# Kernel tuning notes

Hardware: AMD Instinct MI355X
Metric: run time of the kernel (lower is better)

Reference implementation:

```python
import jax, jax.numpy as jnp
import numpy as np
from jax import lax

ITERATIONS = 10
B, I, D, J, E = 512, 7, 512, 64, 128


def setup_inputs() -> dict:
    key = jax.random.key(0)
    k1, k2, k3 = jax.random.split(key, 3)
    f_bid = jax.random.normal(k1, (B, I, D), dtype=jnp.float32)
    p_bi = jax.random.uniform(k2, (B, I), dtype=jnp.float32)
    weights = jax.random.normal(k3, (I, D, J, E), dtype=jnp.float32)
    return {"f_bid": f_bid, "p_bi": p_bi, "weights": weights}


def reference(f_bid, p_bi, weights):
    # Precompute the per-capsule vote tensor once: [B, I, J, E]
    f_W_bije = jnp.einsum('bid,idje->bije', f_bid, weights)
    b = f_bid.shape[0]
    j, e = weights.shape[2], weights.shape[3]
    c0 = jnp.ones((b, j, e), dtype=f_bid.dtype)

    def body(c_bj, _):
        # routing logits over output capsules j, softmax over j (dim=-1 of 'bij')
        r_bij = jax.nn.softmax(jnp.einsum('bije,bje->bij', f_W_bije, c_bj), axis=-1)
        c_next = jnp.einsum('bi,bij,bije->bje', p_bi, r_bij, f_W_bije)
        return c_next, r_bij

    c_bj, r_stack = lax.scan(body, c0, None, length=ITERATIONS)
    return c_bj, r_stack[-1]
```

## Files before the change

### kernel.cpp

```cpp
#include <hip/hip_runtime.h>
#include <hip/hip_bf16.h>

#define B_SZ 512
#define I_SZ 7
#define D_SZ 512
#define J_SZ 64
#define E_SZ 128
#define N_SZ 8192
#define ITERS 10

typedef __attribute__((ext_vector_type(8))) short bf16x8;
typedef __attribute__((ext_vector_type(4))) float f32x4;

#define AST 40
#define BST 40

#if defined(__has_builtin)
#if __has_builtin(__builtin_amdgcn_cvt_pk_bf16_f32)
#define HAVE_CVT_PK_BF16 1
#endif
#endif

__device__ inline void split2(float x0, float x1, unsigned& hp, unsigned& lp) {
#ifdef HAVE_CVT_PK_BF16
    auto h = __builtin_amdgcn_cvt_pk_bf16_f32(x0, x1);
    hp = __builtin_bit_cast(unsigned, h);
    union { unsigned u; float f; } b0, b1;
    b0.u = hp << 16;
    b1.u = hp & 0xFFFF0000u;
    auto l = __builtin_amdgcn_cvt_pk_bf16_f32(x0 - b0.f, x1 - b1.f);
    lp = __builtin_bit_cast(unsigned, l);
#else
    union { float f; unsigned u; } u0, u1;
    u0.f = x0; u1.f = x1;
    unsigned r0 = u0.u + 0x7FFF + ((u0.u >> 16) & 1);
    unsigned r1 = u1.u + 0x7FFF + ((u1.u >> 16) & 1);
    hp = __builtin_amdgcn_perm(r1, r0, 0x07060302);
    union { unsigned u; float f; } h0, h1;
    h0.u = r0 & 0xFFFF0000u;
    h1.u = r1 & 0xFFFF0000u;
    union { float f; unsigned u; } s0, s1;
    s0.f = x0 - h0.f; s1.f = x1 - h1.f;
    unsigned q0 = s0.u + 0x7FFF + ((s0.u >> 16) & 1);
    unsigned q1 = s1.u + 0x7FFF + ((s1.u >> 16) & 1);
    lp = __builtin_amdgcn_perm(q1, q0, 0x07060302);
#endif
}

__global__ __launch_bounds__(256) void vote_gemm_mfma(
    const float* __restrict__ f,
    const float* __restrict__ W,
    float* __restrict__ fW)
{
    const int i  = blockIdx.z;
    const int m0 = blockIdx.y * 128;
    const int n0 = blockIdx.x * 128;
    const int th = threadIdx.x;

    __shared__ short As_hi[128 * AST], As_lo[128 * AST];
    __shared__ short Bs_hi[128 * BST], Bs_lo[128 * BST];

    const int am  = th >> 1;
    const int akg = th & 1;
    const int bn  = th & 127;
    const int bkh = th >> 7;

    const float* fA = f + (size_t)(m0 + am) * (I_SZ * D_SZ) + (size_t)i * D_SZ + akg * 16;
    const float* WB = W + (size_t)i * D_SZ * N_SZ + n0 + bn;

    const int wave = th >> 6, lane = th & 63;
    const int wr = wave >> 1, wc = wave & 1;
    const int lm = lane & 15, quad = lane >> 4;

    f32x4 acc[4][4];
#pragma unroll
    for (int a = 0; a < 4; ++a)
#pragma unroll
        for (int c = 0; c < 4; ++c)
            acc[a][c] = (f32x4){0.f, 0.f, 0.f, 0.f};

    float av[16], bv[16];
    {
        float4 t0 = *(const float4*)(fA);
        float4 t1 = *(const float4*)(fA + 4);
        float4 t2 = *(const float4*)(fA + 8);
        float4 t3 = *(const float4*)(fA + 12);
        av[0]=t0.x; av[1]=t0.y; av[2]=t0.z; av[3]=t0.w;
        av[4]=t1.x; av[5]=t1.y; av[6]=t1.z; av[7]=t1.w;
        av[8]=t2.x; av[9]=t2.y; av[10]=t2.z; av[11]=t2.w;
        av[12]=t3.x; av[13]=t3.y; av[14]=t3.z; av[15]=t3.w;
        const float* pb = WB + (size_t)(bkh * 16) * N_SZ;
#pragma unroll
        for (int r = 0; r < 16; ++r) bv[r] = pb[(size_t)r * N_SZ];
    }

    for (int k0 = 0; k0 < D_SZ; k0 += 32) {
        uint4 ah0, al0, ah1, al1, bh0, bl0, bh1, bl1;
        split2(av[0],  av[1],  ah0.x, al0.x);
        split2(av[2],  av[3],  ah0.y, al0.y);
        split2(av[4],  av[5],  ah0.z, al0.z);
        split2(av[6],  av[7],  ah0.w, al0.w);
        split2(av[8],  av[9],  ah1.x, al1.x);
        split2(av[10], av[11], ah1.y, al1.y);
        split2(av[12], av[13], ah1.z, al1.z);
        split2(av[14], av[15], ah1.w, al1.w);
        split2(bv[0],  bv[1],  bh0.x, bl0.x);
        split2(bv[2],  bv[3],  bh0.y, bl0.y);
        split2(bv[4],  bv[5],  bh0.z, bl0.z);
        split2(bv[6],  bv[7],  bh0.w, bl0.w);
        split2(bv[8],  bv[9],  bh1.x, bl1.x);
        split2(bv[10], bv[11], bh1.y, bl1.y);
        split2(bv[12], bv[13], bh1.z, bl1.z);
        split2(bv[14], bv[15], bh1.w, bl1.w);

        __syncthreads();
        *(uint4*)&As_hi[am * AST + akg * 16]     = ah0;
        *(uint4*)&As_hi[am * AST + akg * 16 + 8] = ah1;
        *(uint4*)&As_lo[am * AST + akg * 16]     = al0;
        *(uint4*)&As_lo[am * AST + akg * 16 + 8] = al1;
        *(uint4*)&Bs_hi[bn * BST + bkh * 16]     = bh0;
        *(uint4*)&Bs_hi[bn * BST + bkh * 16 + 8] = bh1;
        *(uint4*)&Bs_lo[bn * BST + bkh * 16]     = bl0;
        *(uint4*)&Bs_lo[bn * BST + bkh * 16 + 8] = bl1;
        __syncthreads();

        if (k0 + 32 < D_SZ) {
            const float* pa = fA + k0 + 32;
            float4 t0 = *(const float4*)(pa);
            float4 t1 = *(const float4*)(pa + 4);
            float4 t2 = *(const float4*)(pa + 8);
            float4 t3 = *(const float4*)(pa + 12);
            av[0]=t0.x; av[1]=t0.y; av[2]=t0.z; av[3]=t0.w;
            av[4]=t1.x; av[5]=t1.y; av[6]=t1.z; av[7]=t1.w;
            av[8]=t2.x; av[9]=t2.y; av[10]=t2.z; av[11]=t2.w;
            av[12]=t3.x; av[13]=t3.y; av[14]=t3.z; av[15]=t3.w;
            const float* pb = WB + (size_t)(k0 + 32 + bkh * 16) * N_SZ;
#pragma unroll
            for (int r = 0; r < 16; ++r) bv[r] = pb[(size_t)r * N_SZ];
        }

        bf16x8 Ah[4], Al[4], Bh[4], Bl[4];
#pragma unroll
        for (int t = 0; t < 4; ++t) {
            const int ar = (wr * 64 + t * 16 + lm) * AST + quad * 8;
            Ah[t] = *(const bf16x8*)&As_hi[ar];
            Al[t] = *(const bf16x8*)&As_lo[ar];
            const int br = (wc * 64 + t * 16 + lm) * BST + quad * 8;
            Bh[t] = *(const bf16x8*)&Bs_hi[br];
            Bl[t] = *(const bf16x8*)&Bs_lo[br];
        }
#pragma unroll
        for (int tm = 0; tm < 4; ++tm)
#pragma unroll
            for (int tn = 0; tn < 4; ++tn) {
                acc[tm][tn] = __builtin_amdgcn_mfma_f32_16x16x32_bf16(Ah[tm], Bh[tn], acc[tm][tn], 0, 0, 0);
                acc[tm][tn] = __builtin_amdgcn_mfma_f32_16x16x32_bf16(Ah[tm], Bl[tn], acc[tm][tn], 0, 0, 0);
                acc[tm][tn] = __builtin_amdgcn_mfma_f32_16x16x32_bf16(Al[tm], Bh[tn], acc[tm][tn], 0, 0, 0);
            }
    }

#pragma unroll
    for (int tm = 0; tm < 4; ++tm) {
        const int rowb = m0 + wr * 64 + tm * 16 + quad * 4;
#pragma unroll
        for (int tn = 0; tn < 4; ++tn) {
            const int col = n0 + wc * 64 + tn * 16 + lm;
#pragma unroll
            for (int r = 0; r < 4; ++r)
                fW[((size_t)(rowb + r) * I_SZ + i) * N_SZ + col] = acc[tm][tn][r];
        }
    }
}

__global__ __launch_bounds__(1024) void routing_kernel(
    const float* __restrict__ fW,
    const float* __restrict__ p,
    float* __restrict__ c_out,
    float* __restrict__ r_out)
{
    const int b   = blockIdx.x;
    const int tid = threadIdx.x;
    const int j   = tid >> 4;
    const int sub = tid & 15;

    __shared__ float G_sh[64][49];
    __shared__ float s_sh[64][9];
    __shared__ float w_sh[2][64][9];
    __shared__ float p_sh[8];

    if (tid < I_SZ) p_sh[tid] = p[(size_t)b * I_SZ + tid];

    float4 fw[I_SZ][2];
    const float* base = fW + (size_t)b * I_SZ * N_SZ + j * E_SZ + sub * 8;
#pragma unroll
    for (int i = 0; i < I_SZ; ++i) {
        fw[i][0] = *(const float4*)(base + (size_t)i * N_SZ);
        fw[i][1] = *(const float4*)(base + (size_t)i * N_SZ + 4);
    }

#pragma unroll
    for (int i = 0; i < I_SZ; ++i) {
        float s = fw[i][0].x + fw[i][0].y + fw[i][0].z + fw[i][0].w
                + fw[i][1].x + fw[i][1].y + fw[i][1].z + fw[i][1].w;
        s += __shfl_xor(s, 1); s += __shfl_xor(s, 2);
        s += __shfl_xor(s, 4); s += __shfl_xor(s, 8);
        if (sub == 0) s_sh[j][i] = s;
#pragma unroll
        for (int i2 = i; i2 < I_SZ; ++i2) {
            float g = fw[i][0].x * fw[i2][0].x + fw[i][0].y * fw[i2][0].y
                    + fw[i][0].z * fw[i2][0].z + fw[i][0].w * fw[i2][0].w
                    + fw[i][1].x * fw[i2][1].x + fw[i][1].y * fw[i2][1].y
                    + fw[i][1].z * fw[i2][1].z + fw[i][1].w * fw[i2][1].w;
            g += __shfl_xor(g, 1); g += __shfl_xor(g, 2);
            g += __shfl_xor(g, 4); g += __shfl_xor(g, 8);
            if (sub == 0) { G_sh[j][i * 7 + i2] = g; G_sh[j][i2 * 7 + i] = g; }
        }
    }
    __syncthreads();

    for (int t = 0; t < ITERS; ++t) {
        if (tid < I_SZ * 64) {
            const int ii = tid >> 6;
            const int jj = tid & 63;
            float l;
            if (t == 0) {
                l = s_sh[jj][ii];
            } else {
                const int rb = t & 1;
                l = 0.f;
#pragma unroll
                for (int i2 = 0; i2 < I_SZ; ++i2)
                    l = fmaf(w_sh[rb][jj][i2], G_sh[jj][ii * 7 + i2], l);
            }
            float mx = l;
#pragma unroll
            for (int off = 32; off > 0; off >>= 1)
                mx = fmaxf(mx, __shfl_xor(mx, off));
            float ex = __expf(l - mx);
            float sm = ex;
#pragma unroll
            for (int off = 32; off > 0; off >>= 1)
                sm += __shfl_xor(sm, off);
            float r = ex / sm;
            if (t == ITERS - 1)
                r_out[(size_t)b * (I_SZ * J_SZ) + ii * 64 + jj] = r;
            w_sh[(t + 1) & 1][jj][ii] = p_sh[ii] * r;
        }
        __syncthreads();
    }

    float4 a0 = make_float4(0.f, 0.f, 0.f, 0.f);
    float4 a1 = make_float4(0.f, 0.f, 0.f, 0.f);
#pragma unroll
    for (int i = 0; i < I_SZ; ++i) {
        float wv = w_sh[ITERS & 1][j][i];
        a0.x = fmaf(wv, fw[i][0].x, a0.x); a0.y = fmaf(wv, fw[i][0].y, a0.y);
        a0.z = fmaf(wv, fw[i][0].z, a0.z); a0.w = fmaf(wv, fw[i][0].w, a0.w);
        a1.x = fmaf(wv, fw[i][1].x, a1.x); a1.y = fmaf(wv, fw[i][1].y, a1.y);
        a1.z = fmaf(wv, fw[i][1].z, a1.z); a1.w = fmaf(wv, fw[i][1].w, a1.w);
    }
    float* dst = c_out + (size_t)b * N_SZ + j * E_SZ + sub * 8;
    *(float4*)(dst)     = a0;
    *(float4*)(dst + 4) = a1;
}

extern "C" void kernel_launch(void* const* d_in, const int* in_sizes, int n_in,
                              void* d_out, int out_size, void* d_ws, size_t ws_size,
                              hipStream_t stream) {
    const float* f = (const float*)d_in[0];
    const float* p = (const float*)d_in[1];
    const float* W = (const float*)d_in[2];
    float* out = (float*)d_out;
    float* fW  = (float*)d_ws;

    vote_gemm_mfma<<<dim3(N_SZ / 128, B_SZ / 128, I_SZ), 256, 0, stream>>>(f, W, fW);
    routing_kernel<<<B_SZ, 1024, 0, stream>>>(fW, p, out, out + (size_t)B_SZ * N_SZ);
}
```

Before: 295.0 us.

## Restructure vote GEMM with direct-to-LDS double-buffered loads and larger tiles

The vote GEMM now stages raw fp32 A and B tiles straight from global memory into LDS with global_load_lds, double-buffered and swizzled to avoid bank conflicts. The bf16 hi/lo split moves to after the LDS reads, and block tiles grow to 256x256 with 512 threads. MFMA sections are wrapped in s_setprio. The goal is to overlap global loads with MFMA work and cut register staging and per-step synchronisation. In exchange, the split is repeated by every wave that reads the same tile, and the grid shrinks to 448 large blocks using about 128KB of LDS each, which risks tail imbalance and low occupancy.

```diff
diff --git a/kernel.cpp b/kernel.cpp
--- a/kernel.cpp
+++ b/kernel.cpp
@@ -11,9 +11,6 @@
 
 typedef __attribute__((ext_vector_type(8))) short bf16x8;
 typedef __attribute__((ext_vector_type(4))) float f32x4;
-
-#define AST 40
-#define BST 40
 
 #if defined(__has_builtin)
 #if __has_builtin(__builtin_amdgcn_cvt_pk_bf16_f32)
@@ -47,127 +44,137 @@
 #endif
 }
 
-__global__ __launch_bounds__(256) void vote_gemm_mfma(
+__device__ inline void gload16(const float* g, float* l) {
+    __builtin_amdgcn_global_load_lds(
+        (const __attribute__((address_space(1))) void*)g,
+        (__attribute__((address_space(3))) void*)l, 16, 0, 0);
+}
+
+__global__ __launch_bounds__(512) void vote_gemm_mfma(
     const float* __restrict__ f,
     const float* __restrict__ W,
     float* __restrict__ fW)
 {
     const int i  = blockIdx.z;
-    const int m0 = blockIdx.y * 128;
-    const int n0 = blockIdx.x * 128;
+    const int m0 = blockIdx.y * 256;
+    const int n0 = blockIdx.x * 256;
     const int th = threadIdx.x;
-
-    __shared__ short As_hi[128 * AST], As_lo[128 * AST];
-    __shared__ short Bs_hi[128 * BST], Bs_lo[128 * BST];
-
-    const int am  = th >> 1;
-    const int akg = th & 1;
-    const int bn  = th & 127;
-    const int bkh = th >> 7;
-
-    const float* fA = f + (size_t)(m0 + am) * (I_SZ * D_SZ) + (size_t)i * D_SZ + akg * 16;
-    const float* WB = W + (size_t)i * D_SZ * N_SZ + n0 + bn;
-
-    const int wave = th >> 6, lane = th & 63;
-    const int wr = wave >> 1, wc = wave & 1;
-    const int lm = lane & 15, quad = lane >> 4;
-
-    f32x4 acc[4][4];
-#pragma unroll
-    for (int a = 0; a < 4; ++a)
+    const int lane = th & 63;
+    const int wave = th >> 6;
+    const int wr  = wave >> 2;
+    const int wc  = wave & 3;
+    const int q   = lane >> 4;
+    const int l15 = lane & 15;
+
+    __shared__ float ldsA[2][256 * 32];
+    __shared__ float ldsB[2][32 * 256];
+
+    const float* aSrc[4];
+    const float* bSrc[4];
+#pragma unroll
+    for (int ci = 0; ci < 4; ++ci) {
+        const int ia = ci * 512 + th;
+        const int mA = ia >> 3, sA = ia & 7;
+        aSrc[ci] = f + (size_t)(m0 + mA) * (I_SZ * D_SZ) + (size_t)i * D_SZ
+                     + ((sA ^ (mA & 7)) << 2);
+        const int ib = ci * 512 + th;
+        const int kB = ib >> 6, cB = ib & 63;
+        bSrc[ci] = W + (size_t)i * D_SZ * N_SZ + (size_t)kB * N_SZ + n0
+                     + ((cB ^ ((kB & 8) >> 1)) << 2);
+    }
+
+    auto stage = [&](int slot) {
+#pragma unroll
+        for (int ci = 0; ci < 4; ++ci)
+            gload16(aSrc[ci], &ldsA[slot][(ci * 512 + th) * 4]);
+#pragma unroll
+        for (int ci = 0; ci < 4; ++ci)
+            gload16(bSrc[ci], &ldsB[slot][(ci * 512 + th) * 4]);
+#pragma unroll
+        for (int ci = 0; ci < 4; ++ci) {
+            aSrc[ci] += 32;
+            bSrc[ci] += (size_t)32 * N_SZ;
+        }
+    };
+
+    f32x4 acc[8][4];
+#pragma unroll
+    for (int a = 0; a < 8; ++a)
 #pragma unroll
         for (int c = 0; c < 4; ++c)
             acc[a][c] = (f32x4){0.f, 0.f, 0.f, 0.f};
 
-    float av[16], bv[16];
-    {
-        float4 t0 = *(const float4*)(fA);
-        float4 t1 = *(const float4*)(fA + 4);
-        float4 t2 = *(const float4*)(fA + 8);
-        float4 t3 = *(const float4*)(fA + 12);
-        av[0]=t0.x; av[1]=t0.y; av[2]=t0.z; av[3]=t0.w;
-        av[4]=t1.x; av[5]=t1.y; av[6]=t1.z; av[7]=t1.w;
-        av[8]=t2.x; av[9]=t2.y; av[10]=t2.z; av[11]=t2.w;
-        av[12]=t3.x; av[13]=t3.y; av[14]=t3.z; av[15]=t3.w;
-        const float* pb = WB + (size_t)(bkh * 16) * N_SZ;
-#pragma unroll
-        for (int r = 0; r < 16; ++r) bv[r] = pb[(size_t)r * N_SZ];
-    }
-
-    for (int k0 = 0; k0 < D_SZ; k0 += 32) {
-        uint4 ah0, al0, ah1, al1, bh0, bl0, bh1, bl1;
-        split2(av[0],  av[1],  ah0.x, al0.x);
-        split2(av[2],  av[3],  ah0.y, al0.y);
-        split2(av[4],  av[5],  ah0.z, al0.z);
-        split2(av[6],  av[7],  ah0.w, al0.w);
-        split2(av[8],  av[9],  ah1.x, al1.x);
-        split2(av[10], av[11], ah1.y, al1.y);
-        split2(av[12], av[13], ah1.z, al1.z);
-        split2(av[14], av[15], ah1.w, al1.w);
-        split2(bv[0],  bv[1],  bh0.x, bl0.x);
-        split2(bv[2],  bv[3],  bh0.y, bl0.y);
-        split2(bv[4],  bv[5],  bh0.z, bl0.z);
-        split2(bv[6],  bv[7],  bh0.w, bl0.w);
-        split2(bv[8],  bv[9],  bh1.x, bl1.x);
-        split2(bv[10], bv[11], bh1.y, bl1.y);
-        split2(bv[12], bv[13], bh1.z, bl1.z);
-        split2(bv[14], bv[15], bh1.w, bl1.w);
-
-        __syncthreads();
-        *(uint4*)&As_hi[am * AST + akg * 16]     = ah0;
-        *(uint4*)&As_hi[am * AST + akg * 16 + 8] = ah1;
-        *(uint4*)&As_lo[am * AST + akg * 16]     = al0;
-        *(uint4*)&As_lo[am * AST + akg * 16 + 8] = al1;
-        *(uint4*)&Bs_hi[bn * BST + bkh * 16]     = bh0;
-        *(uint4*)&Bs_hi[bn * BST + bkh * 16 + 8] = bh1;
-        *(uint4*)&Bs_lo[bn * BST + bkh * 16]     = bl0;
-        *(uint4*)&Bs_lo[bn * BST + bkh * 16 + 8] = bl1;
-        __syncthreads();
-
-        if (k0 + 32 < D_SZ) {
-            const float* pa = fA + k0 + 32;
-            float4 t0 = *(const float4*)(pa);
-            float4 t1 = *(const float4*)(pa + 4);
-            float4 t2 = *(const float4*)(pa + 8);
-            float4 t3 = *(const float4*)(pa + 12);
-            av[0]=t0.x; av[1]=t0.y; av[2]=t0.z; av[3]=t0.w;
-            av[4]=t1.x; av[5]=t1.y; av[6]=t1.z; av[7]=t1.w;
-            av[8]=t2.x; av[9]=t2.y; av[10]=t2.z; av[11]=t2.w;
-            av[12]=t3.x; av[13]=t3.y; av[14]=t3.z; av[15]=t3.w;
-            const float* pb = WB + (size_t)(k0 + 32 + bkh * 16) * N_SZ;
-#pragma unroll
-            for (int r = 0; r < 16; ++r) bv[r] = pb[(size_t)r * N_SZ];
-        }
-
-        bf16x8 Ah[4], Al[4], Bh[4], Bl[4];
-#pragma unroll
-        for (int t = 0; t < 4; ++t) {
-            const int ar = (wr * 64 + t * 16 + lm) * AST + quad * 8;
-            Ah[t] = *(const bf16x8*)&As_hi[ar];
-            Al[t] = *(const bf16x8*)&As_lo[ar];
-            const int br = (wc * 64 + t * 16 + lm) * BST + quad * 8;
-            Bh[t] = *(const bf16x8*)&Bs_hi[br];
-            Bl[t] = *(const bf16x8*)&Bs_lo[br];
-        }
-#pragma unroll
-        for (int tm = 0; tm < 4; ++tm)
-#pragma unroll
-            for (int tn = 0; tn < 4; ++tn) {
-                acc[tm][tn] = __builtin_amdgcn_mfma_f32_16x16x32_bf16(Ah[tm], Bh[tn], acc[tm][tn], 0, 0, 0);
-                acc[tm][tn] = __builtin_amdgcn_mfma_f32_16x16x32_bf16(Ah[tm], Bl[tn], acc[tm][tn], 0, 0, 0);
-                acc[tm][tn] = __builtin_amdgcn_mfma_f32_16x16x32_bf16(Al[tm], Bh[tn], acc[tm][tn], 0, 0, 0);
+    stage(0);
+    stage(1);
+    asm volatile("s_waitcnt vmcnt(8)" ::: "memory");
+    __builtin_amdgcn_s_barrier();
+    asm volatile("" ::: "memory");
+
+    for (int t = 0; t < 16; ++t) {
+        const int slot = t & 1;
+        const float* Ab = &ldsA[slot][0];
+        const float* Bb = &ldsB[slot][0];
+
+        uint4 Bh4[4], Bl4[4];
+#pragma unroll
+        for (int ns = 0; ns < 4; ++ns) {
+            const int cs = (wc * 16 + ns * 4 + (l15 >> 2)) ^ ((q & 1) << 2);
+            const float* bp = Bb + q * 8 * 256 + cs * 4 + (l15 & 3);
+            const float b0 = bp[0 * 256], b1 = bp[1 * 256], b2 = bp[2 * 256], b3 = bp[3 * 256];
+            const float b4 = bp[4 * 256], b5 = bp[5 * 256], b6 = bp[6 * 256], b7 = bp[7 * 256];
+            split2(b0, b1, Bh4[ns].x, Bl4[ns].x);
+            split2(b2, b3, Bh4[ns].y, Bl4[ns].y);
+            split2(b4, b5, Bh4[ns].z, Bl4[ns].z);
+            split2(b6, b7, Bh4[ns].w, Bl4[ns].w);
+        }
+
+#pragma unroll
+        for (int ms = 0; ms < 8; ++ms) {
+            const int mrow = wr * 128 + ms * 16 + l15;
+            const int p0 = (q * 2) ^ (l15 & 7);
+            const float4 va = *(const float4*)(Ab + mrow * 32 + ((p0 ^ 0) << 2));
+            const float4 vb = *(const float4*)(Ab + mrow * 32 + ((p0 ^ 1) << 2));
+            uint4 ah, al;
+            split2(va.x, va.y, ah.x, al.x);
+            split2(va.z, va.w, ah.y, al.y);
+            split2(vb.x, vb.y, ah.z, al.z);
+            split2(vb.z, vb.w, ah.w, al.w);
+            const bf16x8 Ah = __builtin_bit_cast(bf16x8, ah);
+            const bf16x8 Al = __builtin_bit_cast(bf16x8, al);
+            __builtin_amdgcn_s_setprio(1);
+#pragma unroll
+            for (int ns = 0; ns < 4; ++ns) {
+                const bf16x8 Bh = __builtin_bit_cast(bf16x8, Bh4[ns]);
+                const bf16x8 Bl = __builtin_bit_cast(bf16x8, Bl4[ns]);
+                acc[ms][ns] = __builtin_amdgcn_mfma_f32_16x16x32_bf16(Ah, Bh, acc[ms][ns], 0, 0, 0);
+                acc[ms][ns] = __builtin_amdgcn_mfma_f32_16x16x32_bf16(Ah, Bl, acc[ms][ns], 0, 0, 0);
+                acc[ms][ns] = __builtin_amdgcn_mfma_f32_16x16x32_bf16(Al, Bh, acc[ms][ns], 0, 0, 0);
             }
-    }
-
-#pragma unroll
-    for (int tm = 0; tm < 4; ++tm) {
-        const int rowb = m0 + wr * 64 + tm * 16 + quad * 4;
-#pragma unroll
-        for (int tn = 0; tn < 4; ++tn) {
-            const int col = n0 + wc * 64 + tn * 16 + lm;
+            __builtin_amdgcn_s_setprio(0);
+        }
+
+        asm volatile("s_waitcnt lgkmcnt(0)" ::: "memory");
+        __builtin_amdgcn_s_barrier();
+        asm volatile("" ::: "memory");
+        if (t < 14) {
+            stage(slot);
+            asm volatile("s_waitcnt vmcnt(8)" ::: "memory");
+        } else {
+            asm volatile("s_waitcnt vmcnt(0)" ::: "memory");
+        }
+        __builtin_amdgcn_s_barrier();
+        asm volatile("" ::: "memory");
+    }
+
+#pragma unroll
+    for (int ms = 0; ms < 8; ++ms) {
+        const int rowb = m0 + wr * 128 + ms * 16 + q * 4;
+#pragma unroll
+        for (int ns = 0; ns < 4; ++ns) {
+            const int col = n0 + wc * 64 + ns * 16 + l15;
 #pragma unroll
             for (int r = 0; r < 4; ++r)
-                fW[((size_t)(rowb + r) * I_SZ + i) * N_SZ + col] = acc[tm][tn][r];
+                fW[((size_t)(rowb + r) * I_SZ + i) * N_SZ + col] = acc[ms][ns][r];
         }
     }
 }
@@ -273,6 +280,6 @@
     float* out = (float*)d_out;
     float* fW  = (float*)d_ws;
 
-    vote_gemm_mfma<<<dim3(N_SZ / 128, B_SZ / 128, I_SZ), 256, 0, stream>>>(f, W, fW);
+    vote_gemm_mfma<<<dim3(N_SZ / 256, B_SZ / 256, I_SZ), 512, 0, stream>>>(f, W, fW);
     routing_kernel<<<B_SZ, 1024, 0, stream>>>(fW, p, out, out + (size_t)B_SZ * N_SZ);
 }
```

Result: slower. 347.1 us (+17.6%).
